# Optimization experiments

Hardware: AMD Instinct MI355X
Metric: run time of the kernel (lower is better)

The kernel has to match this reference:

```python
import jax, jax.numpy as jnp
import numpy as np

B, S, D, L = 4, 2048, 1024, 4  # batch, seq_len, d_model, num_layers


def setup_inputs() -> dict:
    key = jax.random.key(0)
    ks = jax.random.split(key, 6)
    w = lambda k, shape: jax.random.normal(k, shape, jnp.float32) * 0.02
    return {
        "x": jax.random.normal(ks[0], (B, S, D), jnp.float32),
        # stacked per-layer parameters [L, ...]
        "Wkqv": w(ks[1], (L, D, 3 * D)),
        "Wm1": w(ks[2], (L, D, 2 * D)), "bm1": jnp.zeros((L, 2 * D), jnp.float32),
        "Wm2": w(ks[3], (L, D, D)), "bm2": jnp.zeros((L, D), jnp.float32),
        "gn_g": jnp.ones((L, D), jnp.float32), "gn_b": jnp.zeros((L, D), jnp.float32),
        "Wf1": w(ks[4], (L, D, 2 * D)), "bf1": jnp.zeros((L, 2 * D), jnp.float32),
        "Wf2": w(ks[5], (L, 2 * D, D)), "bf2": jnp.zeros((L, D), jnp.float32),
        "ln_g": jnp.ones((L, D), jnp.float32), "ln_b": jnp.zeros((L, D), jnp.float32),
    }


def _retention(x, wkqv):
    d = x.shape[-1]
    k, q, v = jnp.split(x @ wkqv, 3, axis=-1)            # each [B,S,D]
    qkt = jnp.einsum('bid,bjd->bij', q, k) / jnp.sqrt(jnp.float32(d))
    s = x.shape[1]
    row_norm = 1.0 + jnp.sqrt(jnp.arange(s, dtype=x.dtype))[None, :, None]
    r = jnp.tril(qkt) / row_norm                          # causal, per-row sqrt-index norm
    denom = jnp.clip(jnp.abs(r.sum(-1, keepdims=True)), 1.0, None)
    r = r / denom
    return jnp.einsum('bij,bjd->bid', r, v)


def _groupnorm1(y, g, b, eps=1e-5):
    # torch GroupNorm(1, D) on [B, D, S]: normalize over (D, S) per batch element
    mu = y.mean(axis=(1, 2), keepdims=True)
    var = y.var(axis=(1, 2), keepdims=True)
    return (y - mu) / jnp.sqrt(var + eps) * g + b


def _layernorm(y, g, b, eps=1e-5):
    mu = y.mean(-1, keepdims=True)
    var = y.var(-1, keepdims=True)
    return (y - mu) / jnp.sqrt(var + eps) * g + b


def reference(x, Wkqv, Wm1, bm1, Wm2, bm2, gn_g, gn_b, Wf1, bf1, Wf2, bf2, ln_g, ln_b):
    def block(h, p):
        wk, w1, b1, w2, b2, gg, gb, wf1, bf1_, wf2, bf2_, lg, lb = p
        r = _retention(h, wk)
        m = r @ w1 + b1
        a, gate = jnp.split(m, 2, axis=-1)                # SwiGLU
        m = (a * jax.nn.silu(gate)) @ w2 + b2
        m = _groupnorm1(m, gg, gb)
        y = m + h
        f = jax.nn.gelu(y @ wf1 + bf1_, approximate=False) @ wf2 + bf2_
        return _layernorm(f + y, lg, lb), None

    params = (Wkqv, Wm1, bm1, Wm2, bm2, gn_g, gn_b, Wf1, bf1, Wf2, bf2, ln_g, ln_b)
    out, _ = jax.lax.scan(block, x, params)
    return out
```

## Files before the change

kernel.cpp:

```cpp
#include <hip/hip_runtime.h>


constexpr int Bb = 4, Ss = 2048, Dd = 1024, Ll = 4;
constexpr int BSm = Bb * Ss;

typedef short bf16x8 __attribute__((ext_vector_type(8)));
typedef float f32x4  __attribute__((ext_vector_type(4)));
typedef unsigned short us;

__device__ __forceinline__ us bf16_rn(float x) {
    unsigned int u = __float_as_uint(x);
    u += 0x7FFFu + ((u >> 16) & 1u);
    return (us)(u >> 16);
}
__device__ __forceinline__ float bf2f(us h) {
    return __uint_as_float(((unsigned int)h) << 16);
}
__device__ __forceinline__ void fsplit(float v, us& h, us& l) {
    h = bf16_rn(v);
    l = bf16_rn(v - bf2f(h));
}

#define GLL(g, l) __builtin_amdgcn_global_load_lds( \
    (const __attribute__((address_space(1))) void*)(g), \
    (__attribute__((address_space(3))) void*)(l), 16, 0, 0)

#define MFMA16(a, b, c) __builtin_amdgcn_mfma_f32_16x16x32_bf16(a, b, c, 0, 0, 0)

template<int OUT, bool HAS_BIAS, int ACT, bool CAUSAL, bool CK, bool ROWSCALE>
__global__ __launch_bounds__(256, 2) void gemm3(
    const us* __restrict__ Ahg, const us* __restrict__ Alg, int lda, long sA,
    const us* __restrict__ Bhg, const us* __restrict__ Blg, int ldb, long sB,
    const float* __restrict__ bias,
    float* __restrict__ Cf, us* __restrict__ Ch, us* __restrict__ Cl,
    int ldc, long sC,
    const float* __restrict__ drec, int K)
{
    __shared__ __align__(16) char lds[2 * 32768];

    if (CAUSAL && blockIdx.x > blockIdx.y) return;
    const int t = threadIdx.x, z = blockIdx.z;
    const int row0 = blockIdx.y * 128, col0 = blockIdx.x * 128;
    Ahg += (size_t)z * sA;  Alg += (size_t)z * sA;
    Bhg += (size_t)z * sB;  Blg += (size_t)z * sB;

    const int srow = t >> 2;
    const int scg  = ((t & 3) ^ ((t >> 3) & 3)) * 8;
    const us* pAh = Ahg + (size_t)(row0 + srow) * lda + scg;
    const us* pAl = Alg + (size_t)(row0 + srow) * lda + scg;
    const us* pBh = Bhg + (size_t)(col0 + srow) * ldb + scg;
    const us* pBl = Blg + (size_t)(col0 + srow) * ldb + scg;
    const size_t a64 = (size_t)64 * lda, b64 = (size_t)64 * ldb;
    const int wb = (t >> 6) * 1024;

    auto stage = [&](int kt) {
        const int k0 = kt * 32;
        char* base = lds + (kt & 1) * 32768 + wb;
        GLL(pAh + k0,       base + 0 * 8192);
        GLL(pAh + k0 + a64, base + 0 * 8192 + 4096);
        GLL(pAl + k0,       base + 1 * 8192);
        GLL(pAl + k0 + a64, base + 1 * 8192 + 4096);
        GLL(pBh + k0,       base + 2 * 8192);
        GLL(pBh + k0 + b64, base + 2 * 8192 + 4096);
        GLL(pBl + k0,       base + 3 * 8192);
        GLL(pBl + k0 + b64, base + 3 * 8192 + 4096);
    };

    const int ln = t & 63, lr = ln & 15, q = ln >> 4;
    const int w  = t >> 6, wm = w >> 1, wn = w & 1;
    const int xq = (q ^ ((lr >> 1) & 3)) * 16;
    int offA[4], offB[4];
    #pragma unroll
    for (int m = 0; m < 4; ++m) offA[m] = (wm * 64 + m * 16 + lr) * 64 + xq;
    #pragma unroll
    for (int n = 0; n < 4; ++n) offB[n] = (wn * 64 + n * 16 + lr) * 64 + xq;

    f32x4 acc[4][4] = {};

    int Keff = K;
    if (CK) { int ke = row0 + 128; Keff = ke < K ? ke : K; }
    const int NT = Keff >> 5;

    stage(0);
    for (int kt = 0; kt < NT; ++kt) {
        __syncthreads();
        if (kt + 1 < NT) stage(kt + 1);
        const char* base = lds + (kt & 1) * 32768;
        bf16x8 ah[4], al8[4], bh[4], bl8[4];
        #pragma unroll
        for (int m = 0; m < 4; ++m) {
            ah[m]  = *reinterpret_cast<const bf16x8*>(base + 0 * 8192 + offA[m]);
            al8[m] = *reinterpret_cast<const bf16x8*>(base + 1 * 8192 + offA[m]);
        }
        #pragma unroll
        for (int n = 0; n < 4; ++n) {
            bh[n]  = *reinterpret_cast<const bf16x8*>(base + 2 * 8192 + offB[n]);
            bl8[n] = *reinterpret_cast<const bf16x8*>(base + 3 * 8192 + offB[n]);
        }
        #pragma unroll
        for (int n = 0; n < 4; ++n) {
            #pragma unroll
            for (int m = 0; m < 4; ++m) acc[m][n] = MFMA16(ah[m],  bh[n],  acc[m][n]);
            #pragma unroll
            for (int m = 0; m < 4; ++m) acc[m][n] = MFMA16(ah[m],  bl8[n], acc[m][n]);
            #pragma unroll
            for (int m = 0; m < 4; ++m) acc[m][n] = MFMA16(al8[m], bh[n],  acc[m][n]);
        }
    }

    const float* dz = drec + (size_t)z * Ss;
    #pragma unroll
    for (int n = 0; n < 4; ++n) {
        const int col = col0 + wn * 64 + n * 16 + lr;
        const float bv = HAS_BIAS ? bias[col] : 0.0f;
        #pragma unroll
        for (int m = 0; m < 4; ++m) {
            #pragma unroll
            for (int j = 0; j < 4; ++j) {
                const int row = row0 + wm * 64 + m * 16 + 4 * q + j;
                float v = acc[m][n][j] + bv;
                if (ACT == 1)
                    v = 0.5f * v * (1.0f + erff(v * 0.70710678118f));
                if (CAUSAL)
                    v = (col <= row)
                        ? v * (1.0f / (32.0f * (1.0f + sqrtf((float)row))))
                        : 0.0f;
                if (ROWSCALE) v *= dz[row];
                const size_t idx = (size_t)z * sC + (size_t)row * ldc + col;
                if (OUT == 0) {
                    Cf[idx] = v;
                } else {
                    us h_, l_;
                    fsplit(v, h_, l_);
                    Ch[idx] = h_;
                    Cl[idx] = l_;
                }
            }
        }
    }
}

__global__ __launch_bounds__(256) void split_k(
    const float* __restrict__ in, us* __restrict__ oh, us* __restrict__ ol)
{
    const size_t e = (size_t)blockIdx.x * 256 + threadIdx.x;
    float4 v = *reinterpret_cast<const float4*>(in + e * 4);
    ushort4 h4, l4;
    fsplit(v.x, h4.x, l4.x); fsplit(v.y, h4.y, l4.y);
    fsplit(v.z, h4.z, l4.z); fsplit(v.w, h4.w, l4.w);
    *reinterpret_cast<ushort4*>(oh + e * 4) = h4;
    *reinterpret_cast<ushort4*>(ol + e * 4) = l4;
}

__global__ __launch_bounds__(256) void tsplit_k(
    const float* __restrict__ in, long sin_,
    us* __restrict__ oh, us* __restrict__ ol, long sout, int H, int W)
{
    __shared__ float tile[32][33];
    const int z = blockIdx.z;
    in += (size_t)z * sin_;  oh += (size_t)z * sout;  ol += (size_t)z * sout;
    const int c0 = blockIdx.x * 32, r0 = blockIdx.y * 32;
    const int tr = threadIdx.x >> 3, tc = (threadIdx.x & 7) * 4;
    float4 v = *reinterpret_cast<const float4*>(in + (size_t)(r0 + tr) * W + c0 + tc);
    tile[tr][tc + 0] = v.x; tile[tr][tc + 1] = v.y;
    tile[tr][tc + 2] = v.z; tile[tr][tc + 3] = v.w;
    __syncthreads();
    ushort4 h4, l4;
    fsplit(tile[tc + 0][tr], h4.x, l4.x);
    fsplit(tile[tc + 1][tr], h4.y, l4.y);
    fsplit(tile[tc + 2][tr], h4.z, l4.z);
    fsplit(tile[tc + 3][tr], h4.w, l4.w);
    const size_t o = (size_t)(c0 + tr) * H + r0 + tc;
    *reinterpret_cast<ushort4*>(oh + o) = h4;
    *reinterpret_cast<ushort4*>(ol + o) = l4;
}

__global__ __launch_bounds__(256) void denom_k(
    const us* __restrict__ sph, const us* __restrict__ spl,
    float* __restrict__ drec)
{
    const int r = blockIdx.x, b = blockIdx.y, t = threadIdx.x;
    const us* ph = sph + ((size_t)b * Ss + r) * Ss;
    const us* pl = spl + ((size_t)b * Ss + r) * Ss;
    const int jmax = ((r >> 7) + 1) << 7;
    float s = 0.f;
    for (int j4 = t; j4 * 4 < jmax; j4 += 256) {
        ushort4 h = *reinterpret_cast<const ushort4*>(ph + j4 * 4);
        ushort4 lo = *reinterpret_cast<const ushort4*>(pl + j4 * 4);
        s += (bf2f(h.x) + bf2f(lo.x)) + (bf2f(h.y) + bf2f(lo.y))
           + (bf2f(h.z) + bf2f(lo.z)) + (bf2f(h.w) + bf2f(lo.w));
    }
    __shared__ float rs[256];
    rs[t] = s;
    __syncthreads();
    for (int off = 128; off > 0; off >>= 1) {
        if (t < off) rs[t] += rs[t + off];
        __syncthreads();
    }
    if (t == 0) drec[(size_t)b * Ss + r] = 1.0f / fmaxf(1.0f, fabsf(rs[0]));
}

__global__ __launch_bounds__(256) void swiglu_k(
    const float* __restrict__ m1, us* __restrict__ oh, us* __restrict__ ol)
{
    const size_t e = (size_t)blockIdx.x * 256 + threadIdx.x;
    const size_t row = e / (Dd / 4);
    const int c4 = (int)(e % (Dd / 4));
    const float* base = m1 + row * (2 * Dd);
    float4 a = *reinterpret_cast<const float4*>(base + c4 * 4);
    float4 g = *reinterpret_cast<const float4*>(base + Dd + c4 * 4);
    float o0 = a.x * (g.x / (1.f + expf(-g.x)));
    float o1 = a.y * (g.y / (1.f + expf(-g.y)));
    float o2 = a.z * (g.z / (1.f + expf(-g.z)));
    float o3 = a.w * (g.w / (1.f + expf(-g.w)));
    ushort4 h4, l4;
    fsplit(o0, h4.x, l4.x); fsplit(o1, h4.y, l4.y);
    fsplit(o2, h4.z, l4.z); fsplit(o3, h4.w, l4.w);
    const size_t o = row * Dd + c4 * 4;
    *reinterpret_cast<ushort4*>(oh + o) = h4;
    *reinterpret_cast<ushort4*>(ol + o) = l4;
}

__global__ __launch_bounds__(256) void gn_part_k(
    const float* __restrict__ m2, float* __restrict__ part)
{
    const int b = blockIdx.y, blk = blockIdx.x;
    const float* p = m2 + (size_t)b * Ss * Dd + (size_t)blk * 8192;
    float s = 0.f, ss = 0.f;
    for (int t = threadIdx.x; t < 2048; t += 256) {
        float4 v = *reinterpret_cast<const float4*>(p + (size_t)t * 4);
        s  += (v.x + v.y) + (v.z + v.w);
        ss += v.x * v.x + v.y * v.y + v.z * v.z + v.w * v.w;
    }
    __shared__ float rs[256], rss[256];
    rs[threadIdx.x] = s; rss[threadIdx.x] = ss;
    __syncthreads();
    for (int off = 128; off > 0; off >>= 1) {
        if (threadIdx.x < off) {
            rs[threadIdx.x]  += rs[threadIdx.x + off];
            rss[threadIdx.x] += rss[threadIdx.x + off];
        }
        __syncthreads();
    }
    if (threadIdx.x == 0) {
        part[(b * 256 + blk) * 2]     = rs[0];
        part[(b * 256 + blk) * 2 + 1] = rss[0];
    }
}

__global__ __launch_bounds__(256) void gn_final_k(
    const float* __restrict__ part, float* __restrict__ stats)
{
    const int b = blockIdx.x, t = threadIdx.x;
    float s  = part[(b * 256 + t) * 2];
    float ss = part[(b * 256 + t) * 2 + 1];
    __shared__ float rs[256], rss[256];
    rs[t] = s; rss[t] = ss;
    __syncthreads();
    for (int off = 128; off > 0; off >>= 1) {
        if (t < off) { rs[t] += rs[t + off]; rss[t] += rss[t + off]; }
        __syncthreads();
    }
    if (t == 0) {
        const float inv_n = 1.0f / (float)((size_t)Ss * Dd);
        float mean = rs[0] * inv_n;
        float var  = fmaxf(rss[0] * inv_n - mean * mean, 0.0f);
        stats[b * 2]     = mean;
        stats[b * 2 + 1] = rsqrtf(var + 1e-5f);
    }
}

__global__ __launch_bounds__(256) void gn_apply_k(
    const float* __restrict__ m2, const float* __restrict__ h,
    const float* __restrict__ g, const float* __restrict__ bta,
    const float* __restrict__ stats, float* __restrict__ y,
    us* __restrict__ yh, us* __restrict__ yl)
{
    const size_t e = (size_t)blockIdx.x * 256 + threadIdx.x;
    const int b  = (int)(e / ((size_t)Ss * Dd / 4));
    const int c4 = (int)(e % (Dd / 4));
    const float mean = stats[b * 2], istd = stats[b * 2 + 1];
    float4 m  = *reinterpret_cast<const float4*>(m2 + e * 4);
    float4 hh = *reinterpret_cast<const float4*>(h + e * 4);
    float4 g4 = *reinterpret_cast<const float4*>(g + c4 * 4);
    float4 b4 = *reinterpret_cast<const float4*>(bta + c4 * 4);
    float4 o;
    o.x = (m.x - mean) * istd * g4.x + b4.x + hh.x;
    o.y = (m.y - mean) * istd * g4.y + b4.y + hh.y;
    o.z = (m.z - mean) * istd * g4.z + b4.z + hh.z;
    o.w = (m.w - mean) * istd * g4.w + b4.w + hh.w;
    *reinterpret_cast<float4*>(y + e * 4) = o;
    ushort4 h4, l4;
    fsplit(o.x, h4.x, l4.x); fsplit(o.y, h4.y, l4.y);
    fsplit(o.z, h4.z, l4.z); fsplit(o.w, h4.w, l4.w);
    *reinterpret_cast<ushort4*>(yh + e * 4) = h4;
    *reinterpret_cast<ushort4*>(yl + e * 4) = l4;
}

template<bool SPLIT>
__global__ __launch_bounds__(256) void ln_k(
    const float* __restrict__ f2, const float* __restrict__ y,
    const float* __restrict__ g, const float* __restrict__ bta,
    float* __restrict__ out, us* __restrict__ oh, us* __restrict__ ol)
{
    const int row = blockIdx.x;
    const int t = threadIdx.x;
    float4 fv = *reinterpret_cast<const float4*>(f2 + (size_t)row * Dd + t * 4);
    float4 yv = *reinterpret_cast<const float4*>(y  + (size_t)row * Dd + t * 4);
    const float v0 = fv.x + yv.x, v1 = fv.y + yv.y;
    const float v2 = fv.z + yv.z, v3 = fv.w + yv.w;
    float s  = (v0 + v1) + (v2 + v3);
    float ss = v0 * v0 + v1 * v1 + v2 * v2 + v3 * v3;
    __shared__ float rs[256], rss[256];
    rs[t] = s; rss[t] = ss;
    __syncthreads();
    for (int off = 128; off > 0; off >>= 1) {
        if (t < off) { rs[t] += rs[t + off]; rss[t] += rss[t + off]; }
        __syncthreads();
    }
    const float mean = rs[0] * (1.0f / Dd);
    const float var  = fmaxf(rss[0] * (1.0f / Dd) - mean * mean, 0.0f);
    const float istd = rsqrtf(var + 1e-5f);
    float4 g4 = *reinterpret_cast<const float4*>(g + t * 4);
    float4 b4 = *reinterpret_cast<const float4*>(bta + t * 4);
    float4 o;
    o.x = (v0 - mean) * istd * g4.x + b4.x;
    o.y = (v1 - mean) * istd * g4.y + b4.y;
    o.z = (v2 - mean) * istd * g4.z + b4.z;
    o.w = (v3 - mean) * istd * g4.w + b4.w;
    *reinterpret_cast<float4*>(out + (size_t)row * Dd + t * 4) = o;
    if (SPLIT) {
        ushort4 h4, l4;
        fsplit(o.x, h4.x, l4.x); fsplit(o.y, h4.y, l4.y);
        fsplit(o.z, h4.z, l4.z); fsplit(o.w, h4.w, l4.w);
        const size_t e = (size_t)row * Dd + t * 4;
        *reinterpret_cast<ushort4*>(oh + e) = h4;
        *reinterpret_cast<ushort4*>(ol + e) = l4;
    }
}

extern "C" void kernel_launch(void* const* d_in, const int* in_sizes, int n_in,
                              void* d_out, int out_size, void* d_ws, size_t ws_size,
                              hipStream_t stream)
{
    const float* x    = (const float*)d_in[0];
    const float* Wkqv = (const float*)d_in[1];
    const float* Wm1  = (const float*)d_in[2];
    const float* bm1  = (const float*)d_in[3];
    const float* Wm2  = (const float*)d_in[4];
    const float* bm2  = (const float*)d_in[5];
    const float* gng  = (const float*)d_in[6];
    const float* gnb  = (const float*)d_in[7];
    const float* Wf1  = (const float*)d_in[8];
    const float* bf1  = (const float*)d_in[9];
    const float* Wf2  = (const float*)d_in[10];
    const float* bf2  = (const float*)d_in[11];
    const float* lng  = (const float*)d_in[12];
    const float* lnb  = (const float*)d_in[13];

    char* wsb = (char*)d_ws;
    const size_t MiB = 1024 * 1024;
    auto SL = [&](int i) { return wsb + (size_t)i * 16 * MiB; };

    float* hbuf   = (float*)SL(0);
    us* h_hi      = (us*)SL(2);
    us* h_lo      = (us*)SL(3);
    us* qk_hi     = (us*)SL(4);
    us* qk_lo     = (us*)SL(6);
    float* vbuf   = (float*)SL(8);
    us* WtA_hi    = (us*)SL(10);
    us* WtA_lo    = (us*)(SL(10) + 6 * MiB);
    us* vT_hi     = (us*)SL(2);
    us* vT_lo     = (us*)SL(3);
    us* sp_hi     = (us*)SL(8);
    us* sp_lo     = (us*)SL(10);
    float* drec   = (float*)SL(4);
    us* ret_hi    = (us*)SL(6);
    us* ret_lo    = (us*)SL(7);
    us* Wt1_hi    = (us*)SL(2);
    us* Wt1_lo    = (us*)(SL(2) + 4 * MiB);
    float* m1     = (float*)SL(8);
    us* sw_hi     = (us*)SL(4);
    us* sw_lo     = (us*)SL(5);
    us* Wt2_hi    = (us*)SL(2);
    us* Wt2_lo    = (us*)(SL(2) + 2 * MiB);
    float* m2     = (float*)SL(10);
    float* part   = (float*)SL(2);
    float* stats  = (float*)(SL(2) + 1 * MiB);
    float* ybuf   = (float*)SL(8);
    us* y_hi      = (us*)SL(4);
    us* y_lo      = (us*)SL(5);
    us* Wtf1_hi   = (us*)SL(6);
    us* Wtf1_lo   = (us*)(SL(6) + 4 * MiB);
    us* f1_hi     = (us*)SL(10);
    us* f1_lo     = (us*)SL(2);
    us* Wtf2_hi   = (us*)SL(6);
    us* Wtf2_lo   = (us*)(SL(6) + 4 * MiB);
    float* f2     = (float*)SL(4);

    for (int l = 0; l < Ll; ++l) {
        const float* h = (l == 0) ? x : hbuf;
        if (l == 0)
            split_k<<<8192, 256, 0, stream>>>(x, h_hi, h_lo);

        tsplit_k<<<dim3(3 * Dd / 32, Dd / 32, 1), 256, 0, stream>>>(
            Wkqv + (size_t)l * Dd * 3 * Dd, 0, WtA_hi, WtA_lo, 0, Dd, 3 * Dd);
        gemm3<1, false, 0, false, false, false><<<dim3(16, 64, 1), 256, 0, stream>>>(
            h_hi, h_lo, Dd, 0, WtA_hi, WtA_lo, Dd, 0, nullptr,
            nullptr, qk_hi, qk_lo, 2 * Dd, 0, drec, Dd);
        gemm3<0, false, 0, false, false, false><<<dim3(8, 64, 1), 256, 0, stream>>>(
            h_hi, h_lo, Dd, 0,
            WtA_hi + (size_t)2 * Dd * Dd, WtA_lo + (size_t)2 * Dd * Dd, Dd, 0,
            nullptr, vbuf, nullptr, nullptr, Dd, 0, drec, Dd);
        tsplit_k<<<dim3(Dd / 32, Ss / 32, Bb), 256, 0, stream>>>(
            vbuf, (long)Ss * Dd, vT_hi, vT_lo, (long)Dd * Ss, Ss, Dd);

        gemm3<1, false, 0, true, false, false><<<dim3(16, 16, Bb), 256, 0, stream>>>(
            qk_hi + Dd, qk_lo + Dd, 2 * Dd, (long)Ss * 2 * Dd,
            qk_hi,      qk_lo,      2 * Dd, (long)Ss * 2 * Dd,
            nullptr, nullptr, sp_hi, sp_lo, Ss, (long)Ss * Ss, drec, Dd);
        denom_k<<<dim3(Ss, Bb), 256, 0, stream>>>(sp_hi, sp_lo, drec);
        gemm3<1, false, 0, false, true, true><<<dim3(8, 16, Bb), 256, 0, stream>>>(
            sp_hi, sp_lo, Ss, (long)Ss * Ss,
            vT_hi, vT_lo, Ss, (long)Dd * Ss,
            nullptr, nullptr, ret_hi, ret_lo, Dd, (long)Ss * Dd, drec, Ss);

        tsplit_k<<<dim3(2 * Dd / 32, Dd / 32, 1), 256, 0, stream>>>(
            Wm1 + (size_t)l * Dd * 2 * Dd, 0, Wt1_hi, Wt1_lo, 0, Dd, 2 * Dd);
        gemm3<0, true, 0, false, false, false><<<dim3(16, 64, 1), 256, 0, stream>>>(
            ret_hi, ret_lo, Dd, 0, Wt1_hi, Wt1_lo, Dd, 0,
            bm1 + (size_t)l * 2 * Dd, m1, nullptr, nullptr, 2 * Dd, 0, drec, Dd);
        swiglu_k<<<8192, 256, 0, stream>>>(m1, sw_hi, sw_lo);
        tsplit_k<<<dim3(Dd / 32, Dd / 32, 1), 256, 0, stream>>>(
            Wm2 + (size_t)l * Dd * Dd, 0, Wt2_hi, Wt2_lo, 0, Dd, Dd);
        gemm3<0, true, 0, false, false, false><<<dim3(8, 64, 1), 256, 0, stream>>>(
            sw_hi, sw_lo, Dd, 0, Wt2_hi, Wt2_lo, Dd, 0,
            bm2 + (size_t)l * Dd, m2, nullptr, nullptr, Dd, 0, drec, Dd);

        gn_part_k<<<dim3(256, Bb), 256, 0, stream>>>(m2, part);
        gn_final_k<<<Bb, 256, 0, stream>>>(part, stats);
        gn_apply_k<<<8192, 256, 0, stream>>>(
            m2, h, gng + (size_t)l * Dd, gnb + (size_t)l * Dd, stats,
            ybuf, y_hi, y_lo);

        tsplit_k<<<dim3(2 * Dd / 32, Dd / 32, 1), 256, 0, stream>>>(
            Wf1 + (size_t)l * Dd * 2 * Dd, 0, Wtf1_hi, Wtf1_lo, 0, Dd, 2 * Dd);
        gemm3<1, true, 1, false, false, false><<<dim3(16, 64, 1), 256, 0, stream>>>(
            y_hi, y_lo, Dd, 0, Wtf1_hi, Wtf1_lo, Dd, 0,
            bf1 + (size_t)l * 2 * Dd,
            nullptr, f1_hi, f1_lo, 2 * Dd, 0, drec, Dd);
        tsplit_k<<<dim3(Dd / 32, 2 * Dd / 32, 1), 256, 0, stream>>>(
            Wf2 + (size_t)l * 2 * Dd * Dd, 0, Wtf2_hi, Wtf2_lo, 0, 2 * Dd, Dd);
        gemm3<0, true, 0, false, false, false><<<dim3(8, 64, 1), 256, 0, stream>>>(
            f1_hi, f1_lo, 2 * Dd, 0, Wtf2_hi, Wtf2_lo, 2 * Dd, 0,
            bf2 + (size_t)l * Dd, f2, nullptr, nullptr, Dd, 0, drec, 2 * Dd);

        if (l == Ll - 1)
            ln_k<false><<<BSm, 256, 0, stream>>>(
                f2, ybuf, lng + (size_t)l * Dd, lnb + (size_t)l * Dd,
                (float*)d_out, nullptr, nullptr);
        else
            ln_k<true><<<BSm, 256, 0, stream>>>(
                f2, ybuf, lng + (size_t)l * Dd, lnb + (size_t)l * Dd,
                hbuf, h_hi, h_lo);
    }
}
```

Before: 3.503 ms.

## Load A fragments directly from global into registers, stage only B in LDS

The GEMM no longer stages the A operand (hi/lo bf16 split) through LDS. Each wave now loads its A fragments straight from global memory into registers, double-buffered across even and odd k-tiles, while only B goes through LDS. This halves the LDS footprint and the LDS read traffic, which could allow more occupancy. In exchange, A rows are read redundantly by the two waves sharing a row block, global loads become uncoalesced 16-byte-per-lane reads, and register pressure rises. The loop is unrolled by two and assumes NT is even.

```diff
diff --git a/kernel.cpp b/kernel.cpp
--- a/kernel.cpp
+++ b/kernel.cpp
@@ -36,7 +36,7 @@
     int ldc, long sC,
     const float* __restrict__ drec, int K)
 {
-    __shared__ __align__(16) char lds[2 * 32768];
+    __shared__ __align__(16) char lds[2 * 16384];
 
     if (CAUSAL && blockIdx.x > blockIdx.y) return;
     const int t = threadIdx.x, z = blockIdx.z;
@@ -46,34 +46,31 @@
 
     const int srow = t >> 2;
     const int scg  = ((t & 3) ^ ((t >> 3) & 3)) * 8;
-    const us* pAh = Ahg + (size_t)(row0 + srow) * lda + scg;
-    const us* pAl = Alg + (size_t)(row0 + srow) * lda + scg;
     const us* pBh = Bhg + (size_t)(col0 + srow) * ldb + scg;
     const us* pBl = Blg + (size_t)(col0 + srow) * ldb + scg;
-    const size_t a64 = (size_t)64 * lda, b64 = (size_t)64 * ldb;
+    const size_t b64 = (size_t)64 * ldb;
     const int wb = (t >> 6) * 1024;
 
-    auto stage = [&](int kt) {
+    auto stageB = [&](int kt) {
         const int k0 = kt * 32;
-        char* base = lds + (kt & 1) * 32768 + wb;
-        GLL(pAh + k0,       base + 0 * 8192);
-        GLL(pAh + k0 + a64, base + 0 * 8192 + 4096);
-        GLL(pAl + k0,       base + 1 * 8192);
-        GLL(pAl + k0 + a64, base + 1 * 8192 + 4096);
-        GLL(pBh + k0,       base + 2 * 8192);
-        GLL(pBh + k0 + b64, base + 2 * 8192 + 4096);
-        GLL(pBl + k0,       base + 3 * 8192);
-        GLL(pBl + k0 + b64, base + 3 * 8192 + 4096);
+        char* base = lds + (kt & 1) * 16384 + wb;
+        GLL(pBh + k0,       base + 0 * 8192);
+        GLL(pBh + k0 + b64, base + 0 * 8192 + 4096);
+        GLL(pBl + k0,       base + 1 * 8192);
+        GLL(pBl + k0 + b64, base + 1 * 8192 + 4096);
     };
 
     const int ln = t & 63, lr = ln & 15, q = ln >> 4;
     const int w  = t >> 6, wm = w >> 1, wn = w & 1;
     const int xq = (q ^ ((lr >> 1) & 3)) * 16;
-    int offA[4], offB[4];
-    #pragma unroll
-    for (int m = 0; m < 4; ++m) offA[m] = (wm * 64 + m * 16 + lr) * 64 + xq;
+    int offB[4];
     #pragma unroll
     for (int n = 0; n < 4; ++n) offB[n] = (wn * 64 + n * 16 + lr) * 64 + xq;
+
+    size_t offAm[4];
+    #pragma unroll
+    for (int m = 0; m < 4; ++m)
+        offAm[m] = (size_t)(row0 + wm * 64 + m * 16 + lr) * lda + q * 8;
 
     f32x4 acc[4][4] = {};
 
@@ -81,31 +78,46 @@
     if (CK) { int ke = row0 + 128; Keff = ke < K ? ke : K; }
     const int NT = Keff >> 5;
 
-    stage(0);
-    for (int kt = 0; kt < NT; ++kt) {
-        __syncthreads();
-        if (kt + 1 < NT) stage(kt + 1);
-        const char* base = lds + (kt & 1) * 32768;
-        bf16x8 ah[4], al8[4], bh[4], bl8[4];
+    bf16x8 ahE[4], alE[4], ahO[4], alO[4];
+
+    auto loadA = [&](int kt, bf16x8 (&ah)[4], bf16x8 (&al)[4]) {
+        const int k0 = kt * 32;
         #pragma unroll
         for (int m = 0; m < 4; ++m) {
-            ah[m]  = *reinterpret_cast<const bf16x8*>(base + 0 * 8192 + offA[m]);
-            al8[m] = *reinterpret_cast<const bf16x8*>(base + 1 * 8192 + offA[m]);
+            ah[m] = *reinterpret_cast<const bf16x8*>(Ahg + offAm[m] + k0);
+            al[m] = *reinterpret_cast<const bf16x8*>(Alg + offAm[m] + k0);
         }
+    };
+
+    auto compute = [&](int kt, const bf16x8 (&ah)[4], const bf16x8 (&al)[4]) {
+        const char* base = lds + (kt & 1) * 16384;
+        bf16x8 bh[4], bl8[4];
         #pragma unroll
         for (int n = 0; n < 4; ++n) {
-            bh[n]  = *reinterpret_cast<const bf16x8*>(base + 2 * 8192 + offB[n]);
-            bl8[n] = *reinterpret_cast<const bf16x8*>(base + 3 * 8192 + offB[n]);
+            bh[n]  = *reinterpret_cast<const bf16x8*>(base + 0 * 8192 + offB[n]);
+            bl8[n] = *reinterpret_cast<const bf16x8*>(base + 1 * 8192 + offB[n]);
         }
         #pragma unroll
         for (int n = 0; n < 4; ++n) {
             #pragma unroll
-            for (int m = 0; m < 4; ++m) acc[m][n] = MFMA16(ah[m],  bh[n],  acc[m][n]);
+            for (int m = 0; m < 4; ++m) acc[m][n] = MFMA16(ah[m], bh[n],  acc[m][n]);
             #pragma unroll
-            for (int m = 0; m < 4; ++m) acc[m][n] = MFMA16(ah[m],  bl8[n], acc[m][n]);
+            for (int m = 0; m < 4; ++m) acc[m][n] = MFMA16(ah[m], bl8[n], acc[m][n]);
             #pragma unroll
-            for (int m = 0; m < 4; ++m) acc[m][n] = MFMA16(al8[m], bh[n],  acc[m][n]);
+            for (int m = 0; m < 4; ++m) acc[m][n] = MFMA16(al[m], bh[n],  acc[m][n]);
         }
+    };
+
+    stageB(0);
+    loadA(0, ahE, alE);
+    for (int kt = 0; kt < NT; kt += 2) {
+        __syncthreads();
+        stageB(kt + 1);
+        loadA(kt + 1, ahO, alO);
+        compute(kt, ahE, alE);
+        __syncthreads();
+        if (kt + 2 < NT) { stageB(kt + 2); loadA(kt + 2, ahE, alE); }
+        compute(kt + 1, ahO, alO);
     }
 
     const float* dz = drec + (size_t)z * Ss;
```

New measurement: 5.481 ms. +56.5%, slower.

## Add 256x256-tile 512-thread split-bf16 GEMM for wide projection GEMMs

Applied to the files above, without the earlier changes.

Adds a new gemm3w kernel that uses 256x256 output tiles with 512 threads (8 waves, each covering a 128x64 sub-tile) and 128 KiB of double-buffered LDS. It replaces the 128x128 gemm3 calls for the QK projection, the Wm1 GEMM and the Wf1 GEMM, all of which have N=2048. The larger tile raises arithmetic intensity and cuts global/LDS traffic per MFMA. In exchange it launches only 256 blocks, which lowers occupancy, raises register pressure and may leave CUs underused on a large GPU.

```diff
diff --git a/kernel.cpp b/kernel.cpp
--- a/kernel.cpp
+++ b/kernel.cpp
@@ -127,6 +127,107 @@
                         : 0.0f;
                 if (ROWSCALE) v *= dz[row];
                 const size_t idx = (size_t)z * sC + (size_t)row * ldc + col;
+                if (OUT == 0) {
+                    Cf[idx] = v;
+                } else {
+                    us h_, l_;
+                    fsplit(v, h_, l_);
+                    Ch[idx] = h_;
+                    Cl[idx] = l_;
+                }
+            }
+        }
+    }
+}
+
+template<int OUT, bool HAS_BIAS, int ACT>
+__global__ __launch_bounds__(512, 2) void gemm3w(
+    const us* __restrict__ Ahg, const us* __restrict__ Alg, int lda,
+    const us* __restrict__ Bhg, const us* __restrict__ Blg, int ldb,
+    const float* __restrict__ bias,
+    float* __restrict__ Cf, us* __restrict__ Ch, us* __restrict__ Cl,
+    int ldc, int K)
+{
+    __shared__ __align__(16) char lds[2 * 65536];
+
+    const int t = threadIdx.x;
+    const int row0 = blockIdx.y * 256, col0 = blockIdx.x * 256;
+
+    const int srow = t >> 2;
+    const int scg  = ((t & 3) ^ ((t >> 3) & 3)) * 8;
+    const us* pAh = Ahg + (size_t)(row0 + srow) * lda + scg;
+    const us* pAl = Alg + (size_t)(row0 + srow) * lda + scg;
+    const us* pBh = Bhg + (size_t)(col0 + srow) * ldb + scg;
+    const us* pBl = Blg + (size_t)(col0 + srow) * ldb + scg;
+    const size_t a128 = (size_t)128 * lda, b128 = (size_t)128 * ldb;
+    const int wb = (t >> 6) * 1024;
+
+    auto stage = [&](int kt) {
+        const int k0 = kt * 32;
+        char* base = lds + (kt & 1) * 65536 + wb;
+        GLL(pAh + k0,        base + 0 * 16384);
+        GLL(pAh + k0 + a128, base + 0 * 16384 + 8192);
+        GLL(pAl + k0,        base + 1 * 16384);
+        GLL(pAl + k0 + a128, base + 1 * 16384 + 8192);
+        GLL(pBh + k0,        base + 2 * 16384);
+        GLL(pBh + k0 + b128, base + 2 * 16384 + 8192);
+        GLL(pBl + k0,        base + 3 * 16384);
+        GLL(pBl + k0 + b128, base + 3 * 16384 + 8192);
+    };
+
+    const int ln = t & 63, lr = ln & 15, q = ln >> 4;
+    const int w  = t >> 6, wm = w >> 2, wn = w & 3;
+    const int xq = (q ^ ((lr >> 1) & 3)) * 16;
+    int offA[8], offB[4];
+    #pragma unroll
+    for (int m = 0; m < 8; ++m)
+        offA[m] = (m * 16 + lr) * 64 + xq + wm * 8192;
+    #pragma unroll
+    for (int n = 0; n < 4; ++n) {
+        const int R = wn * 64 + n * 16 + lr;
+        offB[n] = (R & 127) * 64 + xq + (R >> 7) * 8192;
+    }
+
+    f32x4 acc[8][4] = {};
+    const int NT = K >> 5;
+
+    stage(0);
+    for (int kt = 0; kt < NT; ++kt) {
+        __syncthreads();
+        if (kt + 1 < NT) stage(kt + 1);
+        const char* base = lds + (kt & 1) * 65536;
+        bf16x8 ah[8], al8[8];
+        #pragma unroll
+        for (int m = 0; m < 8; ++m) {
+            ah[m]  = *reinterpret_cast<const bf16x8*>(base + 0 * 16384 + offA[m]);
+            al8[m] = *reinterpret_cast<const bf16x8*>(base + 1 * 16384 + offA[m]);
+        }
+        #pragma unroll
+        for (int n = 0; n < 4; ++n) {
+            bf16x8 bh  = *reinterpret_cast<const bf16x8*>(base + 2 * 16384 + offB[n]);
+            bf16x8 bl8 = *reinterpret_cast<const bf16x8*>(base + 3 * 16384 + offB[n]);
+            #pragma unroll
+            for (int m = 0; m < 8; ++m) acc[m][n] = MFMA16(ah[m],  bh,  acc[m][n]);
+            #pragma unroll
+            for (int m = 0; m < 8; ++m) acc[m][n] = MFMA16(ah[m],  bl8, acc[m][n]);
+            #pragma unroll
+            for (int m = 0; m < 8; ++m) acc[m][n] = MFMA16(al8[m], bh,  acc[m][n]);
+        }
+    }
+
+    #pragma unroll
+    for (int n = 0; n < 4; ++n) {
+        const int col = col0 + wn * 64 + n * 16 + lr;
+        const float bv = HAS_BIAS ? bias[col] : 0.0f;
+        #pragma unroll
+        for (int m = 0; m < 8; ++m) {
+            #pragma unroll
+            for (int j = 0; j < 4; ++j) {
+                const int row = row0 + wm * 128 + m * 16 + 4 * q + j;
+                float v = acc[m][n][j] + bv;
+                if (ACT == 1)
+                    v = 0.5f * v * (1.0f + erff(v * 0.70710678118f));
+                const size_t idx = (size_t)row * ldc + col;
                 if (OUT == 0) {
                     Cf[idx] = v;
                 } else {
@@ -405,9 +506,9 @@
 
         tsplit_k<<<dim3(3 * Dd / 32, Dd / 32, 1), 256, 0, stream>>>(
             Wkqv + (size_t)l * Dd * 3 * Dd, 0, WtA_hi, WtA_lo, 0, Dd, 3 * Dd);
-        gemm3<1, false, 0, false, false, false><<<dim3(16, 64, 1), 256, 0, stream>>>(
-            h_hi, h_lo, Dd, 0, WtA_hi, WtA_lo, Dd, 0, nullptr,
-            nullptr, qk_hi, qk_lo, 2 * Dd, 0, drec, Dd);
+        gemm3w<1, false, 0><<<dim3(8, 32), 512, 0, stream>>>(
+            h_hi, h_lo, Dd, WtA_hi, WtA_lo, Dd, nullptr,
+            nullptr, qk_hi, qk_lo, 2 * Dd, Dd);
         gemm3<0, false, 0, false, false, false><<<dim3(8, 64, 1), 256, 0, stream>>>(
             h_hi, h_lo, Dd, 0,
             WtA_hi + (size_t)2 * Dd * Dd, WtA_lo + (size_t)2 * Dd * Dd, Dd, 0,
@@ -427,9 +528,9 @@
 
         tsplit_k<<<dim3(2 * Dd / 32, Dd / 32, 1), 256, 0, stream>>>(
             Wm1 + (size_t)l * Dd * 2 * Dd, 0, Wt1_hi, Wt1_lo, 0, Dd, 2 * Dd);
-        gemm3<0, true, 0, false, false, false><<<dim3(16, 64, 1), 256, 0, stream>>>(
-            ret_hi, ret_lo, Dd, 0, Wt1_hi, Wt1_lo, Dd, 0,
-            bm1 + (size_t)l * 2 * Dd, m1, nullptr, nullptr, 2 * Dd, 0, drec, Dd);
+        gemm3w<0, true, 0><<<dim3(8, 32), 512, 0, stream>>>(
+            ret_hi, ret_lo, Dd, Wt1_hi, Wt1_lo, Dd,
+            bm1 + (size_t)l * 2 * Dd, m1, nullptr, nullptr, 2 * Dd, Dd);
         swiglu_k<<<8192, 256, 0, stream>>>(m1, sw_hi, sw_lo);
         tsplit_k<<<dim3(Dd / 32, Dd / 32, 1), 256, 0, stream>>>(
             Wm2 + (size_t)l * Dd * Dd, 0, Wt2_hi, Wt2_lo, 0, Dd, Dd);
@@ -445,10 +546,10 @@
 
         tsplit_k<<<dim3(2 * Dd / 32, Dd / 32, 1), 256, 0, stream>>>(
             Wf1 + (size_t)l * Dd * 2 * Dd, 0, Wtf1_hi, Wtf1_lo, 0, Dd, 2 * Dd);
-        gemm3<1, true, 1, false, false, false><<<dim3(16, 64, 1), 256, 0, stream>>>(
-            y_hi, y_lo, Dd, 0, Wtf1_hi, Wtf1_lo, Dd, 0,
+        gemm3w<1, true, 1><<<dim3(8, 32), 512, 0, stream>>>(
+            y_hi, y_lo, Dd, Wtf1_hi, Wtf1_lo, Dd,
             bf1 + (size_t)l * 2 * Dd,
-            nullptr, f1_hi, f1_lo, 2 * Dd, 0, drec, Dd);
+            nullptr, f1_hi, f1_lo, 2 * Dd, Dd);
         tsplit_k<<<dim3(Dd / 32, 2 * Dd / 32, 1), 256, 0, stream>>>(
             Wf2 + (size_t)l * 2 * Dd * Dd, 0, Wtf2_hi, Wtf2_lo, 0, 2 * Dd, Dd);
         gemm3<0, true, 0, false, false, false><<<dim3(8, 64, 1), 256, 0, stream>>>(
```

New measurement: 3.318 ms. 1.06x faster.
